# Kernel optimization log

Hardware: AMD Instinct MI355X
Metric: run time of the kernel (lower is better)

Reference implementation:

```python
import jax, jax.numpy as jnp
import numpy as np

B, C, H, W = 8, 256, 64, 64
S = 2            # area_size = sqrt(num_areas)
A = S * S        # num_areas
NH = 8           # num_heads (hardcoded in module)
EPS = 1e-5       # nn.LayerNorm default eps


def setup_inputs() -> dict:
    key = jax.random.key(0)
    ks = jax.random.split(key, 4)
    scale = 0.02
    return {
        "x": jax.random.normal(ks[0], (B, C, H, W), jnp.float32),
        "W_in": jax.random.normal(ks[1], (A, 3 * C, C), jnp.float32) * scale,
        "b_in": jnp.zeros((A, 3 * C), jnp.float32),
        "W_out": jax.random.normal(ks[2], (A, C, C), jnp.float32) * scale,
        "b_out": jnp.zeros((A, C), jnp.float32),
        "gamma": jnp.ones((C,), jnp.float32),
        "beta": jnp.zeros((C,), jnp.float32),
    }


def reference(x, W_in, b_in, W_out, b_out, gamma, beta):
    b, c, h, w = x.shape
    ah, aw = h // S, w // S
    L = ah * aw
    dh = c // NH

    # split into 2x2 areas, flatten each to a sequence: [B, A, L, C]
    # area index = i*S + j (row-major), matching the torch loop order
    xa = (x.reshape(b, c, S, ah, S, aw)
            .transpose(0, 2, 4, 3, 5, 1)   # [B, i, j, ah, aw, C]
            .reshape(b, A, L, c))

    # per-area in-projection (torch Linear: y = x @ W^T + b)
    qkv = jnp.einsum('balc,adc->bald', xa, W_in) + b_in[None, :, None, :]
    q, k, v = jnp.split(qkv, 3, axis=-1)
    q = q.reshape(b, A, L, NH, dh)
    k = k.reshape(b, A, L, NH, dh)
    v = v.reshape(b, A, L, NH, dh)

    scale = jnp.asarray(dh, x.dtype) ** -0.5
    scores = jnp.einsum('balhd,bamhd->bahlm', q * scale, k)  # [B,A,NH,L,L]
    attn = jax.nn.softmax(scores, axis=-1)
    o = jnp.einsum('bahlm,bamhd->balhd', attn, v).reshape(b, A, L, c)
    o = jnp.einsum('balc,adc->bald', o, W_out) + b_out[None, :, None, :]

    # residual + shared LayerNorm over channel dim
    y = o + xa
    mu = jnp.mean(y, axis=-1, keepdims=True)
    var = jnp.mean((y - mu) ** 2, axis=-1, keepdims=True)
    y = (y - mu) * jax.lax.rsqrt(var + EPS) * gamma + beta

    # reassemble areas back to [B, C, H, W]
    out = (y.reshape(b, S, S, ah, aw, c)
             .transpose(0, 5, 1, 3, 2, 4)  # [B, C, i, ah, j, aw]
             .reshape(b, c, h, w))
    return out
```

## Files before the change

### kernel.cpp

```cpp
#include <hip/hip_runtime.h>
#include <cstdint>
#include <cstddef>

#define B_    8
#define C_    256
#define H_    64
#define W_    64
#define A_    4
#define NH_   8
#define DH_   32
#define L_    1024
#define NPAIR 32
#define QKVN  768

typedef __bf16 bf16;
typedef __bf16 bf16x8 __attribute__((ext_vector_type(8)));
typedef __bf16 bf16x4 __attribute__((ext_vector_type(4)));
typedef float  f32x4  __attribute__((ext_vector_type(4)));

#define QSCALE 0.25506866729736328f

__device__ inline f32x4 mfma16(bf16x8 a, bf16x8 b, f32x4 c) {
    return __builtin_amdgcn_mfma_f32_16x16x32_bf16(a, b, c, 0, 0, 0);
}
__device__ inline bf16x8 ld8(const bf16* p) { return *(const bf16x8*)p; }

__device__ inline void stage16(const bf16* g, bf16* l) {
    __builtin_amdgcn_global_load_lds(
        (const __attribute__((address_space(1))) void*)g,
        (__attribute__((address_space(3))) void*)l, 16, 0, 0);
}

#define NW4 (786432 / 4)
#define NO4 (262144 / 4)
__global__ __launch_bounds__(256) void k_split(const float* __restrict__ x,
                                               bf16* __restrict__ xa,
                                               const float* __restrict__ Win,
                                               const float* __restrict__ Wout,
                                               bf16* __restrict__ Winb,
                                               bf16* __restrict__ Woutb) {
    __shared__ float lds[32][257];
    int bid = blockIdx.x;
    int t = threadIdx.x;
    if (bid >= NPAIR * 32) {
        int tid = (bid - NPAIR * 32) * 256 + t;
        if (tid < NW4) {
            float4 v = ((const float4*)Win)[tid];
            bf16x4 ov = {(bf16)v.x, (bf16)v.y, (bf16)v.z, (bf16)v.w};
            ((bf16x4*)Winb)[tid] = ov;
        } else if (tid < NW4 + NO4) {
            int t2 = tid - NW4;
            float4 v = ((const float4*)Wout)[t2];
            bf16x4 ov = {(bf16)v.x, (bf16)v.y, (bf16)v.z, (bf16)v.w};
            ((bf16x4*)Woutb)[t2] = ov;
        }
        return;
    }
    int pair = bid >> 5, p = bid & 31;
    int b = pair >> 2, a = pair & 3, i = a >> 1, j = a & 1;
    int q = t & 31, csub = t >> 5;
    const float* xb = x + (size_t)b * C_ * H_ * W_ + (size_t)(i * 32 + p) * W_ + j * 32;
    for (int r = 0; r < 32; ++r) {
        int c = r * 8 + csub;
        lds[q][c] = xb[(size_t)c * H_ * W_ + q];
    }
    __syncthreads();
    bf16* xr = xa + ((size_t)pair * L_ + (size_t)p * 32) * C_;
    for (int r = 0; r < 32; ++r) {
        xr[(size_t)r * C_ + t] = (bf16)lds[r][t];
    }
}

__global__ __launch_bounds__(256) void k_qkv(const bf16* __restrict__ xa,
                                             const bf16* __restrict__ Win,
                                             const float* __restrict__ bin,
                                             bf16* __restrict__ qk,
                                             bf16* __restrict__ vT) {
    __shared__ __align__(16) char smem[32768];
    bf16* lA = (bf16*)smem;
    bf16* lB = (bf16*)(smem + 16384);
    int bid = blockIdx.x;
    int nt = bid % 6, mt = (bid / 6) & 7, pair = bid / 48;
    int a = pair & 3;
    int t = threadIdx.x, w = t >> 6, lane = t & 63;
    int wm = w >> 1, wn = w & 1;
    int quad = lane >> 4, l16 = lane & 15;
    int m0 = mt * 128, n0 = nt * 128;
    int r8 = lane >> 3, pc = lane & 7, jj = pc ^ r8;
    const bf16* ga = xa + (size_t)pair * L_ * C_ + (size_t)(m0 + w * 32 + r8) * C_ + jj * 8;
    const bf16* gb = Win + (size_t)a * QKVN * C_ + (size_t)(n0 + w * 32 + r8) * C_ + jj * 8;
    f32x4 acc[4][4];
#pragma unroll
    for (int fm = 0; fm < 4; ++fm)
#pragma unroll
        for (int fn = 0; fn < 4; ++fn) acc[fm][fn] = (f32x4){0.f, 0.f, 0.f, 0.f};
#pragma unroll
    for (int i = 0; i < 4; ++i) {
        stage16(ga + (size_t)(i * 8) * C_, lA + (w * 32 + i * 8) * 64);
        stage16(gb + (size_t)(i * 8) * C_, lB + (w * 32 + i * 8) * 64);
    }
    for (int k0 = 0; k0 < C_; k0 += 64) {
        __syncthreads();
        bf16x8 am[2][4], bn[2][4];
#pragma unroll
        for (int ks = 0; ks < 2; ++ks) {
            int p = (ks * 4 + quad) ^ (l16 & 7);
#pragma unroll
            for (int f = 0; f < 4; ++f) {
                am[ks][f] = *(const bf16x8*)&lA[(wm * 64 + f * 16 + l16) * 64 + p * 8];
                bn[ks][f] = *(const bf16x8*)&lB[(wn * 64 + f * 16 + l16) * 64 + p * 8];
            }
        }
        __syncthreads();
        if (k0 + 64 < C_) {
            int kn = k0 + 64;
#pragma unroll
            for (int i = 0; i < 4; ++i) {
                stage16(ga + (size_t)(i * 8) * C_ + kn, lA + (w * 32 + i * 8) * 64);
                stage16(gb + (size_t)(i * 8) * C_ + kn, lB + (w * 32 + i * 8) * 64);
            }
        }
#pragma unroll
        for (int ks = 0; ks < 2; ++ks)
#pragma unroll
            for (int fm = 0; fm < 4; ++fm)
#pragma unroll
                for (int fn = 0; fn < 4; ++fn)
                    acc[fm][fn] = mfma16(am[ks][fm], bn[ks][fn], acc[fm][fn]);
    }
    int colbase = n0 + wn * 64;
    int mb = m0 + wm * 64;
    __syncthreads();
    bf16* slab = (bf16*)smem + w * 2304;
    float bias[4];
#pragma unroll
    for (int fn = 0; fn < 4; ++fn) bias[fn] = bin[a * QKVN + colbase + fn * 16 + l16];
    int sr = lane >> 3, seg = lane & 7;
    if (colbase < 512) {
        float sc = (colbase < 256) ? QSCALE : 1.0f;
        bf16* ob = qk + (size_t)pair * L_ * 512;
#pragma unroll
        for (int pass = 0; pass < 2; ++pass) {
#pragma unroll
            for (int k = 0; k < 2; ++k) {
                int fm = pass * 2 + k;
#pragma unroll
                for (int fn = 0; fn < 4; ++fn)
#pragma unroll
                    for (int r = 0; r < 4; ++r)
                        slab[(k * 16 + quad * 4 + r) * 72 + fn * 16 + l16] =
                            (bf16)((acc[fm][fn][r] + bias[fn]) * sc);
            }
#pragma unroll
            for (int rr = 0; rr < 4; ++rr) {
                int row = rr * 8 + sr;
                bf16x8 v = *(const bf16x8*)&slab[row * 72 + seg * 8];
                *(bf16x8*)&ob[(size_t)(mb + pass * 32 + row) * 512 + colbase + seg * 8] = v;
            }
        }
    } else {
        bf16* vb = vT + (size_t)pair * C_ * L_;
        int e00 = colbase - 512;
#pragma unroll
        for (int pass = 0; pass < 2; ++pass) {
#pragma unroll
            for (int k = 0; k < 2; ++k) {
                int fn = pass * 2 + k;
#pragma unroll
                for (int fm = 0; fm < 4; ++fm) {
                    bf16x4 pk = {(bf16)(acc[fm][fn][0] + bias[fn]), (bf16)(acc[fm][fn][1] + bias[fn]),
                                 (bf16)(acc[fm][fn][2] + bias[fn]), (bf16)(acc[fm][fn][3] + bias[fn])};
                    *(bf16x4*)&slab[(k * 16 + l16) * 72 + fm * 16 + quad * 4] = pk;
                }
            }
#pragma unroll
            for (int rr = 0; rr < 4; ++rr) {
                int el = rr * 8 + sr;
                bf16x8 v = *(const bf16x8*)&slab[el * 72 + seg * 8];
                *(bf16x8*)&vb[(size_t)(e00 + pass * 32 + el) * L_ + mb + seg * 8] = v;
            }
        }
    }
}

__global__ __launch_bounds__(256) void k_attn(const bf16* __restrict__ qk,
                                              const bf16* __restrict__ vT,
                                              bf16* __restrict__ o) {
    __shared__ __align__(16) bf16 pl[4][1024];
    __shared__ __align__(16) bf16 klds[4 * 512];
    __shared__ __align__(16) bf16 vlds[4 * 512];
    int bid = blockIdx.x;
    int pair = bid & 31, rest = bid >> 5;
    int head = rest & 7, qb = rest >> 3;
    int t = threadIdx.x, w = t >> 6, lane = t & 63, quad = lane >> 4, l16 = lane & 15;
    const bf16* qbp = qk + (size_t)pair * L_ * 512;
    const bf16* kg = qbp + (size_t)(l16 * 4 + w) * 512 + 256 + head * DH_ + quad * 8;
    const bf16* vg = vT + ((size_t)pair * C_ + head * DH_ + (w & 1) * 16 + l16) * L_
                        + (w >> 1) * 32 + quad * 8;
    bf16* kdst = &klds[w * 512];
    bf16* vdst = &vlds[w * 512];
    int qbase = qb * 128 + w * 32;
    bf16x8 qf[2];
    f32x4 acc0[2], acc1[2], l4[2];
#pragma unroll
    for (int f = 0; f < 2; ++f) {
        qf[f] = ld8(qbp + (size_t)(qbase + f * 16 + l16) * 512 + head * DH_ + quad * 8);
        acc0[f] = (f32x4){0.f, 0.f, 0.f, 0.f};
        acc1[f] = (f32x4){0.f, 0.f, 0.f, 0.f};
        l4[f]   = (f32x4){0.f, 0.f, 0.f, 0.f};
    }
    stage16(kg, kdst);
    stage16(vg, vdst);
    __syncthreads();

    for (int kv0 = 0; kv0 < L_; kv0 += 64) {
        bf16x8 kf[4], vf[4];
#pragma unroll
        for (int i = 0; i < 4; ++i) {
            kf[i] = ld8(&klds[(i * 64 + lane) * 8]);
            vf[i] = ld8(&vlds[(i * 64 + lane) * 8]);
        }
        __syncthreads();
        int kvn = (kv0 + 64) & (L_ - 1);
        stage16(kg + (size_t)kvn * 512, kdst);
        stage16(vg + kvn, vdst);
#pragma unroll
        for (int f = 0; f < 2; ++f) {
            f32x4 s[4];
#pragma unroll
            for (int kb = 0; kb < 4; ++kb) s[kb] = mfma16(qf[f], kf[kb], (f32x4){0.f, 0.f, 0.f, 0.f});
            char* pw = (char*)&pl[w][0];
#pragma unroll
            for (int r = 0; r < 4; ++r) {
                float p0 = __builtin_amdgcn_exp2f(s[0][r]);
                float p1 = __builtin_amdgcn_exp2f(s[1][r]);
                float p2 = __builtin_amdgcn_exp2f(s[2][r]);
                float p3 = __builtin_amdgcn_exp2f(s[3][r]);
                l4[f][r] += (p0 + p1) + (p2 + p3);
                bf16x4 pv = {(bf16)p0, (bf16)p1, (bf16)p2, (bf16)p3};
                int row = quad * 4 + r;
                int wo = (row * 128 + l16 * 8) ^ ((row & 7) << 4);
                *(bf16x4*)(pw + wo) = pv;
            }
#pragma unroll
            for (int ks = 0; ks < 2; ++ks) {
                int ro = (l16 * 128 + ks * 64 + quad * 16) ^ ((l16 & 7) << 4);
                bf16x8 pf = *(const bf16x8*)(pw + ro);
                acc0[f] = mfma16(pf, vf[ks * 2 + 0], acc0[f]);
                acc1[f] = mfma16(pf, vf[ks * 2 + 1], acc1[f]);
            }
        }
        __syncthreads();
    }
    bf16* orow = o + (size_t)pair * L_ * C_ + head * DH_;
#pragma unroll
    for (int f = 0; f < 2; ++f) {
#pragma unroll
        for (int r = 0; r < 4; ++r) {
            float s1 = l4[f][r];
#pragma unroll
            for (int off = 1; off < 16; off <<= 1) s1 += __shfl_xor(s1, off);
            float inv = 1.f / s1;
            int row = qbase + f * 16 + quad * 4 + r;
            orow[(size_t)row * C_ + l16]      = (bf16)(acc0[f][r] * inv);
            orow[(size_t)row * C_ + 16 + l16] = (bf16)(acc1[f][r] * inv);
        }
    }
}

__global__ __launch_bounds__(256) void k_out(const bf16* __restrict__ o,
                                             const bf16* __restrict__ Wout,
                                             const float* __restrict__ bout,
                                             const bf16* __restrict__ xa,
                                             const float* __restrict__ gamma,
                                             const float* __restrict__ beta,
                                             float* __restrict__ out) {
    __shared__ float tr[32 * 258];
    __shared__ float red[2][2][16][2];
    int bid = blockIdx.x;
    int mt = bid & 31, pair = bid >> 5;
    int a = pair & 3;
    int t = threadIdx.x, w = t >> 6, lane = t & 63;
    int wm = w >> 1, wn = w & 1;
    int quad = lane >> 4, l16 = lane & 15;
    int m0 = mt * 32;
    const bf16* ga = o + (size_t)pair * L_ * C_ + (size_t)(m0 + wm * 16 + l16) * C_;
    const bf16* gb = Wout + (size_t)a * C_ * C_ + (size_t)(wn * 128 + l16) * C_;
    f32x4 acc[8];
#pragma unroll
    for (int fn = 0; fn < 8; ++fn) acc[fn] = (f32x4){0.f, 0.f, 0.f, 0.f};
#pragma unroll 1
    for (int k0 = 0; k0 < C_; k0 += 64) {
#pragma unroll
        for (int ks = 0; ks < 2; ++ks) {
            int kk = k0 + ks * 32 + quad * 8;
            bf16x8 am = ld8(ga + kk);
            bf16x8 bn[8];
#pragma unroll
            for (int f = 0; f < 8; ++f)
                bn[f] = ld8(gb + (size_t)(f * 16) * C_ + kk);
#pragma unroll
            for (int fn = 0; fn < 8; ++fn)
                acc[fn] = mfma16(am, bn[fn], acc[fn]);
        }
    }
    const bf16* xb = xa + ((size_t)pair * L_ + m0 + wm * 16) * C_;
    float g8[8], be8[8];
#pragma unroll
    for (int fn = 0; fn < 8; ++fn) {
        int col = wn * 128 + fn * 16 + l16;
        float bias = bout[a * C_ + col];
        g8[fn] = gamma[col];
        be8[fn] = beta[col];
#pragma unroll
        for (int r = 0; r < 4; ++r)
            acc[fn][r] += bias + (float)xb[(size_t)(quad * 4 + r) * C_ + col];
    }
#pragma unroll
    for (int r = 0; r < 4; ++r) {
        float s1 = 0.f, s2 = 0.f;
#pragma unroll
        for (int fn = 0; fn < 8; ++fn) {
            float v = acc[fn][r];
            s1 += v; s2 += v * v;
        }
#pragma unroll
        for (int off = 1; off < 16; off <<= 1) {
            s1 += __shfl_xor(s1, off);
            s2 += __shfl_xor(s2, off);
        }
        if (l16 == 0) {
            red[wm][wn][quad * 4 + r][0] = s1;
            red[wm][wn][quad * 4 + r][1] = s2;
        }
    }
    __syncthreads();
#pragma unroll
    for (int r = 0; r < 4; ++r) {
        int rl = quad * 4 + r;
        float t1 = red[wm][0][rl][0] + red[wm][1][rl][0];
        float t2 = red[wm][0][rl][1] + red[wm][1][rl][1];
        float mu = t1 * (1.f / 256.f);
        float var = t2 * (1.f / 256.f) - mu * mu;
        float rstd = rsqrtf(var + 1e-5f);
#pragma unroll
        for (int fn = 0; fn < 8; ++fn) {
            float v = (acc[fn][r] - mu) * rstd * g8[fn] + be8[fn];
            tr[(wm * 16 + rl) * 258 + wn * 128 + fn * 16 + l16] = v;
        }
    }
    __syncthreads();
    int b = pair >> 2, i = (a >> 1), j = a & 1;
    int q = t & 31, csub = t >> 5;
    float* ob = out + (size_t)b * C_ * H_ * W_ + (size_t)(i * 32 + mt) * W_ + j * 32;
#pragma unroll
    for (int r32 = 0; r32 < 32; ++r32) {
        int c = r32 * 8 + csub;
        ob[(size_t)c * (H_ * W_) + q] = tr[q * 258 + c];
    }
}

extern "C" void kernel_launch(void* const* d_in, const int* in_sizes, int n_in,
                              void* d_out, int out_size, void* d_ws, size_t ws_size,
                              hipStream_t stream) {
    (void)in_sizes; (void)n_in; (void)out_size; (void)ws_size;
    const float* x     = (const float*)d_in[0];
    const float* Win   = (const float*)d_in[1];
    const float* bin   = (const float*)d_in[2];
    const float* Wout  = (const float*)d_in[3];
    const float* bout  = (const float*)d_in[4];
    const float* gamma = (const float*)d_in[5];
    const float* beta  = (const float*)d_in[6];
    float* out = (float*)d_out;

    char* ws = (char*)d_ws;
    bf16* xa    = (bf16*)ws;
    bf16* qk    = (bf16*)(ws + ((size_t)16 << 20));
    bf16* vT    = (bf16*)(ws + ((size_t)48 << 20));
    bf16* o     = (bf16*)(ws + ((size_t)64 << 20));
    bf16* Winb  = (bf16*)(ws + ((size_t)80 << 20));
    bf16* Woutb = (bf16*)(ws + ((size_t)82 << 20));

    k_split<<<NPAIR * 32 + 1024, 256, 0, stream>>>(x, xa, Win, Wout, Winb, Woutb);
    k_qkv<<<NPAIR * 8 * 6, 256, 0, stream>>>(xa, Winb, bin, qk, vT);
    k_attn<<<NPAIR * NH_ * 8, 256, 0, stream>>>(qk, vT, o);
    k_out<<<NPAIR * 32, 256, 0, stream>>>(o, Woutb, bout, xa, gamma, beta, out);
}
```

Before: 214.9 us.

## Stage out-projection A and B tiles through swizzled LDS in k_out

The out-projection GEMM now copies each 64-wide K slice of the attention output and W_out into shared memory with an XOR swizzle (stage16). Fragments are then read from LDS instead of per-wave global loads, and the next slice is issued before the MFMAs run. The goal is to share W_out rows across the two M waves, coalesce global reads, and overlap loading with compute. It adds two barriers per K step and enlarges shared memory, which aliases the LayerNorm transpose buffer.

```diff
diff --git a/kernel.cpp b/kernel.cpp
--- a/kernel.cpp
+++ b/kernel.cpp
@@ -275,7 +275,10 @@
                                              const float* __restrict__ gamma,
                                              const float* __restrict__ beta,
                                              float* __restrict__ out) {
-    __shared__ float tr[32 * 258];
+    __shared__ __align__(16) char smem[36864];
+    bf16* lA = (bf16*)smem;
+    bf16* lB = (bf16*)(smem + 4096);
+    float* tr = (float*)smem;
     __shared__ float red[2][2][16][2];
     int bid = blockIdx.x;
     int mt = bid & 31, pair = bid >> 5;
@@ -284,25 +287,40 @@
     int wm = w >> 1, wn = w & 1;
     int quad = lane >> 4, l16 = lane & 15;
     int m0 = mt * 32;
-    const bf16* ga = o + (size_t)pair * L_ * C_ + (size_t)(m0 + wm * 16 + l16) * C_;
-    const bf16* gb = Wout + (size_t)a * C_ * C_ + (size_t)(wn * 128 + l16) * C_;
+    int r8 = lane >> 3, pc = lane & 7, jj = pc ^ r8;
+    const bf16* ga = o + (size_t)pair * L_ * C_ + (size_t)(m0 + w * 8 + r8) * C_ + jj * 8;
+    const bf16* gb = Wout + (size_t)a * C_ * C_ + (size_t)(w * 64 + r8) * C_ + jj * 8;
     f32x4 acc[8];
 #pragma unroll
     for (int fn = 0; fn < 8; ++fn) acc[fn] = (f32x4){0.f, 0.f, 0.f, 0.f};
-#pragma unroll 1
+    stage16(ga, lA + (w * 8) * 64);
+#pragma unroll
+    for (int i = 0; i < 8; ++i)
+        stage16(gb + (size_t)(i * 8) * C_, lB + (w * 64 + i * 8) * 64);
     for (int k0 = 0; k0 < C_; k0 += 64) {
+        __syncthreads();
+        bf16x8 am[2], bn[2][8];
 #pragma unroll
         for (int ks = 0; ks < 2; ++ks) {
-            int kk = k0 + ks * 32 + quad * 8;
-            bf16x8 am = ld8(ga + kk);
-            bf16x8 bn[8];
+            int p = (ks * 4 + quad) ^ (l16 & 7);
+            am[ks] = *(const bf16x8*)&lA[(wm * 16 + l16) * 64 + p * 8];
 #pragma unroll
             for (int f = 0; f < 8; ++f)
-                bn[f] = ld8(gb + (size_t)(f * 16) * C_ + kk);
+                bn[ks][f] = *(const bf16x8*)&lB[(wn * 128 + f * 16 + l16) * 64 + p * 8];
+        }
+        __syncthreads();
+        if (k0 + 64 < C_) {
+            int kn = k0 + 64;
+            stage16(ga + kn, lA + (w * 8) * 64);
+#pragma unroll
+            for (int i = 0; i < 8; ++i)
+                stage16(gb + (size_t)(i * 8) * C_ + kn, lB + (w * 64 + i * 8) * 64);
+        }
+#pragma unroll
+        for (int ks = 0; ks < 2; ++ks)
 #pragma unroll
             for (int fn = 0; fn < 8; ++fn)
-                acc[fn] = mfma16(am, bn[fn], acc[fn]);
-        }
+                acc[fn] = mfma16(am[ks], bn[ks][fn], acc[fn]);
     }
     const bf16* xb = xa + ((size_t)pair * L_ + m0 + wm * 16) * C_;
     float g8[8], be8[8];
```

Result: faster. 196.5 us (-8.6%).
